# Kernel optimization log

Measured on AMD Instinct MI355X. Metric: run time of the kernel, lower is better.

## Reference

```python
import jax, jax.numpy as jnp
import numpy as np

T_MAX = 4
TOP_K = 4
TEMP = 1.0
THRESH = 0.99
EPS = 1e-6


def _to_c(x):
    return x[..., 0] + 1j * x[..., 1]


def _from_c(z):
    return jnp.stack([z.real, z.imag], axis=-1)


def _forward(psi, bank_keys, bank_vals, u_halt, W_halt, b_halt, head_mix, out_scale):
    B, T, d, _ = psi.shape
    H = bank_keys.shape[0]
    psi_flat = psi.reshape(B * T, d, 2)
    BT = psi_flat.shape[0]
    psi_h = jnp.broadcast_to(psi_flat[:, None], (BT, H, d, 2))
    cum = jnp.zeros((BT, H), psi.dtype)
    halted = jnp.zeros((BT, H), bool)
    cost = jnp.zeros((BT, H), psi.dtype)
    acc = jnp.zeros((BT, H, d, 2), psi.dtype)
    # normalized halt target vectors u (OrthoHalt)
    uc = _to_c(u_halt)  # [H,d] complex
    un = uc / jnp.sqrt(jnp.sum(uc.real**2 + uc.imag**2, -1, keepdims=True) + EPS)
    hidx = jnp.arange(H)
    for it in range(T_MAX):  # fixed small reasoning depth (structural loop)
        is_last = it == T_MAX - 1
        psi_pool = psi_h.mean(axis=1)                       # [BT,d,2]
        feat = psi_pool.reshape(BT, 2 * d)
        # effect-bank probe + top-k gather
        scores = jnp.einsum('bf,hnf->bhn', feat, bank_keys) / TEMP
        w = jax.nn.softmax(scores, axis=-1)                 # [BT,H,N]
        topw, topi = jax.lax.top_k(w, TOP_K)                # [BT,H,K]
        vecs = bank_vals[hidx[None, :, None], topi]         # [BT,H,K,d,2]
        U = _to_c(vecs) * topw[..., None].astype(jnp.complex64)  # weighted basis
        # rank-K Sasaki projection: Pi_F psi = A (A^H A)^{-1} A^H psi, A = U^T
        psic = _to_c(psi_h)                                 # [BT,H,d]
        m = jnp.einsum('bhkd,bhd->bhk', jnp.conj(U), psic)
        G = jnp.einsum('bhkd,bhjd->bhkj', jnp.conj(U), U)
        G = G + EPS * jnp.eye(TOP_K, dtype=G.dtype)
        coeff = jnp.linalg.solve(G, m[..., None])[..., 0]
        proj = jnp.einsum('bhkd,bhk->bhd', U, coeff)
        psi_next = _from_c(proj)
        # renormalize_psi
        sq = (psi_next[..., 0] ** 2 + psi_next[..., 1] ** 2).sum(-1, keepdims=True)
        psi_next = psi_next / jnp.sqrt(jnp.maximum(sq, 1e-6))[..., None]
        # OrthoHalt on pooled next state -> (alpha, beta, gamma) -> 3 logits
        pool_next = _to_c(psi_next.mean(axis=1))            # [BT,d]
        c = jnp.einsum('hd,bd->bh', jnp.conj(un), pool_next)
        ns = jnp.sum(pool_next.real**2 + pool_next.imag**2, -1)[:, None] + EPS
        alpha = (c.real**2 + c.imag**2) / ns
        beta = 1.0 - alpha
        gamma = c.real**2 / ns
        abg = jnp.stack([alpha, beta, gamma], -1)           # [BT,H,3]
        logits = jnp.einsum('bhi,hij->bhj', abg, W_halt) + b_halt
        probs = jax.nn.softmax(logits, -1)
        p_halt = probs[..., 0] + probs[..., 1]              # yes + no mass
        # ACT ponder update
        would = cum + p_halt
        halts_now = jnp.logical_or(would >= THRESH, is_last)
        active = jnp.logical_not(halted)
        weight = jnp.where(active, jnp.where(halts_now, 1.0 - cum, p_halt), 0.0)
        cost = cost + jnp.where(active, p_halt, 0.0)
        cum = jnp.where(jnp.logical_and(active, jnp.logical_not(halts_now)), would, cum)
        halted = jnp.logical_or(halted, jnp.logical_and(active, halts_now))
        acc = acc + weight[..., None, None] * psi_next
        psi_h = psi_next
    head_w = jax.nn.softmax(head_mix)[None, :, None, None]
    merged = (acc * head_w).sum(axis=1)                     # [BT,d,2]
    residual = merged - psi_flat
    psi_out = (psi_flat + out_scale * residual).reshape(B, T, d, 2)
    return psi_out, cost.mean()


def setup_inputs() -> dict:
    key = jax.random.key(0)
    ks = jax.random.split(key, 6)
    B, T, d, H, N = 2, 2048, 512, 4, 2048
    psi = jax.random.normal(ks[0], (B, T, d, 2), jnp.float32)
    psi = psi / jnp.sqrt(jnp.maximum((psi**2).sum((-1, -2), keepdims=True), 1e-6))
    bank_keys = 0.05 * jax.random.normal(ks[1], (H, N, 2 * d), jnp.float32)
    bank_vals = jax.random.normal(ks[2], (H, N, d, 2), jnp.float32)
    u_halt = jax.random.normal(ks[3], (H, d, 2), jnp.float32)
    W_halt = jax.random.normal(ks[4], (H, 3, 3), jnp.float32)
    b_halt = jnp.zeros((H, 3), jnp.float32)
    head_mix = jnp.zeros((H,), jnp.float32)
    out_scale = jnp.asarray(0.1, jnp.float32)
    return dict(psi=psi, bank_keys=bank_keys, bank_vals=bank_vals, u_halt=u_halt,
                W_halt=W_halt, b_halt=b_halt, head_mix=head_mix, out_scale=out_scale)


def reference(psi, bank_keys, bank_vals, u_halt, W_halt, b_halt, head_mix, out_scale):
    return _forward(psi, bank_keys, bank_vals, u_halt, W_halt, b_halt, head_mix, out_scale)
```

## Files before the change

kernel.cpp:

```cpp
#include <hip/hip_runtime.h>
#include <math.h>

#define HH 4
#define DD 512
#define FF 1024
#define NN 2048
#define KK 4
#define TMAXI 4
#define THRESHV 0.99f
#define EPSV 1e-6f

typedef unsigned short ushort_t;
typedef __attribute__((ext_vector_type(8))) __bf16 bf16x8;
typedef __attribute__((ext_vector_type(4))) float f32x4;
typedef __attribute__((ext_vector_type(4))) unsigned short us4;

__device__ __forceinline__ unsigned short f2bf(float x) {
    unsigned int u = __float_as_uint(x);
    unsigned int r = (u + 0x7FFF + ((u >> 16) & 1)) >> 16;
    return (unsigned short)r;
}

typedef __attribute__((address_space(3))) unsigned int lds_u32;
typedef __attribute__((address_space(1))) const unsigned int glb_u32;
__device__ __forceinline__ void gl_lds16(const void* g, void* s) {
    __builtin_amdgcn_global_load_lds((glb_u32*)g, (lds_u32*)s, 16, 0, 0);
}

__global__ void k_unorm(const float* __restrict__ u_halt, float* __restrict__ norm_inv) {
    __shared__ float red[256];
    int tid = threadIdx.x;
    for (int h = 0; h < HH; ++h) {
        float s = 0.f;
        for (int i = tid; i < FF; i += 256) { float v = u_halt[h * FF + i]; s += v * v; }
        red[tid] = s; __syncthreads();
        for (int off = 128; off > 0; off >>= 1) {
            if (tid < off) red[tid] += red[tid + off];
            __syncthreads();
        }
        if (tid == 0) norm_inv[h] = 1.0f / sqrtf(red[0] + EPSV);
        __syncthreads();
    }
}

__global__ void k_cvt_bf(const float* __restrict__ in, ushort_t* __restrict__ out, int total) {
    int i = blockIdx.x * 256 + threadIdx.x;
    if (i >= total) return;
    out[i] = f2bf(in[i]);
}

#define BM 128
#define BN 128
#define BKE 64
__global__ __launch_bounds__(256) void k_gemm_mfma(const ushort_t* __restrict__ A,
                                                   const ushort_t* __restrict__ B,
                                                   float* __restrict__ C) {
    __shared__ __align__(16) ushort_t As[BM * BKE];
    __shared__ __align__(16) ushort_t Bs[BN * BKE];
    int tid = threadIdx.x;
    int lane = tid & 63, w = tid >> 6;
    int row0 = blockIdx.y * BM, col0 = blockIdx.x * BN;

    int srow = lane >> 3;
    int schunk = (lane & 7) ^ srow;
    const ushort_t* gA = A + (size_t)(row0 + w * 32 + srow) * FF + schunk * 8;
    const ushort_t* gB = B + (size_t)(col0 + w * 32 + srow) * FF + schunk * 8;
    ushort_t* sA = As + (w * 32) * BKE;
    ushort_t* sB = Bs + (w * 32) * BKE;

    int fr = lane & 15;
    int q  = lane >> 4;
    int wr0 = (w >> 1) * 64, wc0 = (w & 1) * 64;

    f32x4 acc[4][4] = {};

    for (int kb = 0; kb < FF; kb += BKE) {
        #pragma unroll
        for (int i = 0; i < 4; i++) {
            gl_lds16(gA + kb + (size_t)(8 * i) * FF, sA + (8 * i) * BKE);
            gl_lds16(gB + kb + (size_t)(8 * i) * FF, sB + (8 * i) * BKE);
        }
        __syncthreads();
        bf16x8 af[2][4], bfv[2][4];
        #pragma unroll
        for (int hf = 0; hf < 2; hf++) {
            int ck = ((4 * hf + q) ^ (fr & 7)) * 8;
            #pragma unroll
            for (int i = 0; i < 4; i++) {
                af[hf][i]  = *(const bf16x8*)&As[(wr0 + 16 * i + fr) * BKE + ck];
                bfv[hf][i] = *(const bf16x8*)&Bs[(wc0 + 16 * i + fr) * BKE + ck];
            }
        }
        #pragma unroll
        for (int hf = 0; hf < 2; hf++)
            #pragma unroll
            for (int i = 0; i < 4; i++)
                #pragma unroll
                for (int j = 0; j < 4; j++)
                    acc[i][j] = __builtin_amdgcn_mfma_f32_16x16x32_bf16(af[hf][i], bfv[hf][j], acc[i][j], 0, 0, 0);
        __syncthreads();
    }

    int crow = (lane >> 4) * 4;
    int ccol = lane & 15;
    #pragma unroll
    for (int i = 0; i < 4; i++)
        #pragma unroll
        for (int r = 0; r < 4; r++) {
            float* Cr = C + (size_t)(row0 + wr0 + 16 * i + crow + r) * (HH * NN) + col0 + wc0 + ccol;
            #pragma unroll
            for (int j = 0; j < 4; j++) Cr[16 * j] = acc[i][j][r];
        }
}

__global__ __launch_bounds__(256) void k_softtop(const float* __restrict__ Sc,
                                                 float* __restrict__ topw, int* __restrict__ topi,
                                                 int row0) {
    int tid = threadIdx.x;
    int w = tid >> 6, lane = tid & 63;
    int g = blockIdx.x * 4 + w;
    int r = g >> 2;
    int h = g & 3;
    const float* S = Sc + (size_t)r * (HH * NN) + h * NN + lane * 4;
    float4 v[8];
    #pragma unroll
    for (int j = 0; j < 8; j++) v[j] = *(const float4*)(S + 256 * j);

    float bm = v[0].x;
    #pragma unroll
    for (int j = 0; j < 8; j++)
        bm = fmaxf(bm, fmaxf(fmaxf(v[j].x, v[j].y), fmaxf(v[j].z, v[j].w)));
    #pragma unroll
    for (int m = 1; m < 64; m <<= 1) bm = fmaxf(bm, __shfl_xor(bm, m, 64));

    float se = 0.f;
    #pragma unroll
    for (int j = 0; j < 8; j++)
        se += __expf(v[j].x - bm) + __expf(v[j].y - bm) + __expf(v[j].z - bm) + __expf(v[j].w - bm);
    #pragma unroll
    for (int m = 1; m < 64; m <<= 1) se += __shfl_xor(se, m, 64);
    float Zinv = __builtin_amdgcn_rcpf(se);

    int gbh = (row0 + r) * HH + h;
    int base = lane * 4;
    #pragma unroll
    for (int k = 0; k < KK; k++) {
        float bv = -INFINITY; int bi = NN;
        #pragma unroll
        for (int j = 0; j < 8; j++) {
            int n0 = 256 * j + base;
            if (v[j].x > bv) { bv = v[j].x; bi = n0; }
            if (v[j].y > bv) { bv = v[j].y; bi = n0 + 1; }
            if (v[j].z > bv) { bv = v[j].z; bi = n0 + 2; }
            if (v[j].w > bv) { bv = v[j].w; bi = n0 + 3; }
        }
        #pragma unroll
        for (int m = 1; m < 64; m <<= 1) {
            float ov = __shfl_xor(bv, m, 64);
            int   oi = __shfl_xor(bi, m, 64);
            if (ov > bv || (ov == bv && oi < bi)) { bv = ov; bi = oi; }
        }
        if (lane == 0) {
            topw[gbh * KK + k] = __expf(bv - bm) * Zinv;
            topi[gbh * KK + k] = bi;
        }
        if (k < KK - 1) {
            #pragma unroll
            for (int j = 0; j < 8; j++) {
                int n0 = 256 * j + base;
                if (n0     == bi) v[j].x = -INFINITY;
                if (n0 + 1 == bi) v[j].y = -INFINITY;
                if (n0 + 2 == bi) v[j].z = -INFINITY;
                if (n0 + 3 == bi) v[j].w = -INFINITY;
            }
        }
    }
}

__global__ __launch_bounds__(256) void k_fused(const float* __restrict__ psi,
                                               float* __restrict__ psi_h,
                                               const float* __restrict__ bank_vals,
                                               const float* __restrict__ topw,
                                               const int* __restrict__ topi,
                                               const float* __restrict__ u_halt,
                                               const float* __restrict__ norm_inv,
                                               const float* __restrict__ W_halt,
                                               const float* __restrict__ b_halt,
                                               const float* __restrict__ head_mix,
                                               float* __restrict__ merged,
                                               ushort_t* __restrict__ feat,
                                               float* __restrict__ cum,
                                               float* __restrict__ cost,
                                               int* __restrict__ halted,
                                               int first, int is_last) {
    __shared__ float Pn[HH][FF];
    __shared__ float xw[4][9];
    int b = blockIdx.x;
    int tid = threadIdx.x;
    int w = tid >> 6, lane = tid & 63;
    int bh = b * HH + w;

    float wk[KK]; int ix[KK];
    #pragma unroll
    for (int k = 0; k < KK; k++) { wk[k] = topw[bh * KK + k]; ix[k] = topi[bh * KK + k]; }

    const float* Pr = first ? (psi + (size_t)b * FF) : (psi_h + (size_t)bh * FF);
    float4 p4[4], v4[KK][4];
    #pragma unroll
    for (int c = 0; c < 4; c++) p4[c] = *(const float4*)(Pr + lane * 16 + 4 * c);
    #pragma unroll
    for (int k = 0; k < KK; k++) {
        const float* Vp = bank_vals + ((size_t)(w * NN) + ix[k]) * FF + lane * 16;
        #pragma unroll
        for (int c = 0; c < 4; c++) v4[k][c] = *(const float4*)(Vp + 4 * c);
    }

    float part[24];
    #pragma unroll
    for (int t = 0; t < 24; t++) part[t] = 0.f;
    #pragma unroll
    for (int c = 0; c < 4; c++) {
        #pragma unroll
        for (int e = 0; e < 2; e++) {
            float prr = e ? p4[c].z : p4[c].x;
            float pii = e ? p4[c].w : p4[c].y;
            float vr[KK], vi[KK];
            #pragma unroll
            for (int k = 0; k < KK; k++) {
                vr[k] = e ? v4[k][c].z : v4[k][c].x;
                vi[k] = e ? v4[k][c].w : v4[k][c].y;
            }
            #pragma unroll
            for (int k = 0; k < KK; k++) {
                part[2 * k]     += vr[k] * prr + vi[k] * pii;
                part[2 * k + 1] += vr[k] * pii - vi[k] * prr;
                part[8 + k]     += vr[k] * vr[k] + vi[k] * vi[k];
            }
            int t = 12;
            #pragma unroll
            for (int k = 0; k < KK; k++)
                #pragma unroll
                for (int j = k + 1; j < KK; j++) {
                    part[t]     += vr[k] * vr[j] + vi[k] * vi[j];
                    part[t + 1] += vr[k] * vi[j] - vi[k] * vr[j];
                    t += 2;
                }
        }
    }
    #pragma unroll
    for (int m = 1; m < 64; m <<= 1)
        #pragma unroll
        for (int t = 0; t < 24; t++) part[t] += __shfl_xor(part[t], m, 64);

    float mr[KK], mi[KK], Gr[KK][KK], Gi[KK][KK];
    #pragma unroll
    for (int k = 0; k < KK; k++) {
        mr[k] = part[2 * k] * wk[k];
        mi[k] = part[2 * k + 1] * wk[k];
        Gr[k][k] = part[8 + k] * wk[k] * wk[k] + EPSV;
        Gi[k][k] = 0.f;
    }
    {
        int t = 12;
        #pragma unroll
        for (int k = 0; k < KK; k++)
            #pragma unroll
            for (int j = k + 1; j < KK; j++) {
                float s = wk[k] * wk[j];
                Gr[k][j] = part[t] * s;  Gi[k][j] = part[t + 1] * s;
                Gr[j][k] = Gr[k][j];     Gi[j][k] = -Gi[k][j];
                t += 2;
            }
    }

    float Lr[KK][KK], Li[KK][KK];
    #pragma unroll
    for (int j = 0; j < KK; j++) {
        float s = Gr[j][j];
        #pragma unroll
        for (int p = 0; p < KK; p++) if (p < j) s -= Lr[j][p] * Lr[j][p] + Li[j][p] * Li[j][p];
        float ljj = sqrtf(fmaxf(s, 1e-30f));
        Lr[j][j] = ljj; Li[j][j] = 0.f;
        float inv = 1.0f / ljj;
        #pragma unroll
        for (int k = 0; k < KK; k++) {
            if (k > j) {
                float ar = Gr[k][j], ai = Gi[k][j];
                #pragma unroll
                for (int p = 0; p < KK; p++) if (p < j) {
                    ar -= Lr[k][p] * Lr[j][p] + Li[k][p] * Li[j][p];
                    ai -= Li[k][p] * Lr[j][p] - Lr[k][p] * Li[j][p];
                }
                Lr[k][j] = ar * inv; Li[k][j] = ai * inv;
            }
        }
    }
    float yr[KK], yi[KK];
    #pragma unroll
    for (int j = 0; j < KK; j++) {
        float ar = mr[j], ai = mi[j];
        #pragma unroll
        for (int p = 0; p < KK; p++) if (p < j) {
            ar -= Lr[j][p] * yr[p] - Li[j][p] * yi[p];
            ai -= Lr[j][p] * yi[p] + Li[j][p] * yr[p];
        }
        float inv = 1.0f / Lr[j][j];
        yr[j] = ar * inv; yi[j] = ai * inv;
    }
    float xr[KK], xi2[KK];
    #pragma unroll
    for (int j = KK - 1; j >= 0; j--) {
        float ar = yr[j], ai = yi[j];
        #pragma unroll
        for (int p = 0; p < KK; p++) if (p > j) {
            ar -= Lr[p][j] * xr[p] + Li[p][j] * xi2[p];
            ai -= Lr[p][j] * xi2[p] - Li[p][j] * xr[p];
        }
        float inv = 1.0f / Lr[j][j];
        xr[j] = ar * inv; xi2[j] = ai * inv;
    }
    float cxr[KK], cxi[KK];
    #pragma unroll
    for (int k = 0; k < KK; k++) { cxr[k] = xr[k] * wk[k]; cxi[k] = xi2[k] * wk[k]; }

    float4 pj[4];
    float sqp = 0.f;
    #pragma unroll
    for (int c = 0; c < 4; c++) {
        float ar0 = 0.f, ai0 = 0.f, ar1 = 0.f, ai1 = 0.f;
        #pragma unroll
        for (int k = 0; k < KK; k++) {
            ar0 += v4[k][c].x * cxr[k] - v4[k][c].y * cxi[k];
            ai0 += v4[k][c].x * cxi[k] + v4[k][c].y * cxr[k];
            ar1 += v4[k][c].z * cxr[k] - v4[k][c].w * cxi[k];
            ai1 += v4[k][c].z * cxi[k] + v4[k][c].w * cxr[k];
        }
        pj[c].x = ar0; pj[c].y = ai0; pj[c].z = ar1; pj[c].w = ai1;
        sqp += ar0 * ar0 + ai0 * ai0 + ar1 * ar1 + ai1 * ai1;
    }
    #pragma unroll
    for (int m = 1; m < 64; m <<= 1) sqp += __shfl_xor(sqp, m, 64);
    float rn = 1.0f / sqrtf(fmaxf(sqp, 1e-6f));

    float* Pdst = psi_h + (size_t)bh * FF + lane * 16;
    #pragma unroll
    for (int c = 0; c < 4; c++) {
        float4 o; o.x = pj[c].x * rn; o.y = pj[c].y * rn; o.z = pj[c].z * rn; o.w = pj[c].w * rn;
        *(float4*)(Pdst + 4 * c) = o;
        *(float4*)&Pn[w][lane * 16 + 4 * c] = o;
    }
    __syncthreads();

    int t4 = tid * 4;
    float4 a0 = *(const float4*)&Pn[0][t4];
    float4 a1 = *(const float4*)&Pn[1][t4];
    float4 a2 = *(const float4*)&Pn[2][t4];
    float4 a3 = *(const float4*)&Pn[3][t4];
    float4 pool;
    pool.x = 0.25f * (a0.x + a1.x + a2.x + a3.x);
    pool.y = 0.25f * (a0.y + a1.y + a2.y + a3.y);
    pool.z = 0.25f * (a0.z + a1.z + a2.z + a3.z);
    pool.w = 0.25f * (a0.w + a1.w + a2.w + a3.w);

    float pt[9];
    #pragma unroll
    for (int h = 0; h < HH; h++) {
        float4 u = *(const float4*)&u_halt[h * FF + t4];
        pt[2 * h]     = u.x * pool.x + u.y * pool.y + u.z * pool.z + u.w * pool.w;
        pt[2 * h + 1] = u.x * pool.y - u.y * pool.x + u.z * pool.w - u.w * pool.z;
    }
    pt[8] = pool.x * pool.x + pool.y * pool.y + pool.z * pool.z + pool.w * pool.w;
    #pragma unroll
    for (int m = 1; m < 64; m <<= 1)
        #pragma unroll
        for (int t = 0; t < 9; t++) pt[t] += __shfl_xor(pt[t], m, 64);
    if (lane == 0) {
        #pragma unroll
        for (int t = 0; t < 9; t++) xw[w][t] = pt[t];
    }
    __syncthreads();
    float red[9];
    #pragma unroll
    for (int t = 0; t < 9; t++) red[t] = xw[0][t] + xw[1][t] + xw[2][t] + xw[3][t];
    float ns = red[8] + EPSV;

    float hm0 = head_mix[0], hm1 = head_mix[1], hm2 = head_mix[2], hm3 = head_mix[3];
    float hmx = fmaxf(fmaxf(hm0, hm1), fmaxf(hm2, hm3));
    float he[4] = {expf(hm0 - hmx), expf(hm1 - hmx), expf(hm2 - hmx), expf(hm3 - hmx)};
    float hsum = he[0] + he[1] + he[2] + he[3];

    float wgt[4], addc[4], newcum[4]; int newhl[4];
    int idxb = b * HH;
    #pragma unroll
    for (int h = 0; h < HH; h++) {
        float cr = red[2 * h] * norm_inv[h], ci = red[2 * h + 1] * norm_inv[h];
        float alpha = (cr * cr + ci * ci) / ns;
        float beta = 1.0f - alpha;
        float gamma = cr * cr / ns;
        float lg[3];
        #pragma unroll
        for (int j = 0; j < 3; j++)
            lg[j] = alpha * W_halt[(h * 3 + 0) * 3 + j] + beta * W_halt[(h * 3 + 1) * 3 + j] +
                    gamma * W_halt[(h * 3 + 2) * 3 + j] + b_halt[h * 3 + j];
        float mx = fmaxf(lg[0], fmaxf(lg[1], lg[2]));
        float e0 = expf(lg[0] - mx), e1 = expf(lg[1] - mx), e2 = expf(lg[2] - mx);
        float p_halt = (e0 + e1) / (e0 + e1 + e2);
        float cm = cum[idxb + h];
        int hl = halted[idxb + h];
        float would = cm + p_halt;
        int halts_now = (would >= THRESHV) || is_last;
        int active = hl ? 0 : 1;
        wgt[h]  = active ? (halts_now ? (1.0f - cm) : p_halt) : 0.0f;
        addc[h] = active ? p_halt : 0.0f;
        newcum[h] = (active && !halts_now) ? would : cm;
        newhl[h]  = hl || (active && halts_now);
    }
    __syncthreads();
    if (tid < HH) {
        cost[idxb + tid] += addc[tid];
        cum[idxb + tid] = newcum[tid];
        halted[idxb + tid] = newhl[tid];
    }
    float hwv[4];
    #pragma unroll
    for (int h = 0; h < HH; h++) hwv[h] = (he[h] / hsum) * wgt[h];

    size_t mo = (size_t)b * FF + t4;
    float4 m4 = *(const float4*)&merged[mo];
    m4.x += hwv[0] * a0.x + hwv[1] * a1.x + hwv[2] * a2.x + hwv[3] * a3.x;
    m4.y += hwv[0] * a0.y + hwv[1] * a1.y + hwv[2] * a2.y + hwv[3] * a3.y;
    m4.z += hwv[0] * a0.z + hwv[1] * a1.z + hwv[2] * a2.z + hwv[3] * a3.z;
    m4.w += hwv[0] * a0.w + hwv[1] * a1.w + hwv[2] * a2.w + hwv[3] * a3.w;
    *(float4*)&merged[mo] = m4;

    us4 fb;
    fb.x = f2bf(pool.x); fb.y = f2bf(pool.y); fb.z = f2bf(pool.z); fb.w = f2bf(pool.w);
    *(us4*)&feat[mo] = fb;
}

__global__ void k_out(const float* __restrict__ psi, const float* __restrict__ merged,
                      const float* __restrict__ out_scale, float* __restrict__ out, int total) {
    int i = blockIdx.x * 256 + threadIdx.x;
    if (i >= total) return;
    float p = psi[i];
    out[i] = p + out_scale[0] * (merged[i] - p);
}

__global__ void k_costmean(const float* __restrict__ cost, float* __restrict__ out, int n) {
    __shared__ float red[256];
    int tid = threadIdx.x;
    float s = 0.f;
    for (int i = tid; i < n; i += 256) s += cost[i];
    red[tid] = s; __syncthreads();
    for (int off = 128; off > 0; off >>= 1) {
        if (tid < off) red[tid] += red[tid + off];
        __syncthreads();
    }
    if (tid == 0) out[0] = red[0] / (float)n;
}

extern "C" void kernel_launch(void* const* d_in, const int* in_sizes, int n_in,
                              void* d_out, int out_size, void* d_ws, size_t ws_size,
                              hipStream_t stream) {
    const float* psi       = (const float*)d_in[0];
    const float* bank_keys = (const float*)d_in[1];
    const float* bank_vals = (const float*)d_in[2];
    const float* u_halt    = (const float*)d_in[3];
    const float* W_halt    = (const float*)d_in[4];
    const float* b_halt    = (const float*)d_in[5];
    const float* head_mix  = (const float*)d_in[6];
    const float* out_scale = (const float*)d_in[7];
    float* out = (float*)d_out;

    const int BT = in_sizes[0] / FF;

    float* ws = (float*)d_ws;
    size_t off = 0;
    float* psi_h  = ws + off; off += (size_t)BT * HH * FF;
    float* merged = ws + off; off += (size_t)BT * FF;
    float* cum    = ws + off; off += (size_t)BT * HH;
    float* costv  = ws + off; off += (size_t)BT * HH;
    int*   halted = (int*)(ws + off); off += (size_t)BT * HH;
    float* topw   = ws + off; off += (size_t)BT * HH * KK;
    int*   topi   = (int*)(ws + off); off += (size_t)BT * HH * KK;
    float* norminv = ws + off; off += 16;
    ushort_t* feat_bf = (ushort_t*)(ws + off); off += (size_t)BT * FF / 2;
    ushort_t* keys_bf = (ushort_t*)(ws + off); off += (size_t)HH * NN * FF / 2;
    float* scores = ws + off;
    size_t fixed = off;

    size_t ws_floats = ws_size / 4;
    int RC = BT;
    while (RC > 128 && fixed + (size_t)RC * HH * NN > ws_floats) RC >>= 1;
    int nchunks = BT / RC;

    hipMemsetAsync(merged, 0, ((size_t)BT * FF + 3 * (size_t)BT * HH) * sizeof(float), stream);
    k_unorm<<<1, 256, 0, stream>>>(u_halt, norminv);
    int tot_keys = HH * NN * FF;
    k_cvt_bf<<<(tot_keys + 255) / 256, 256, 0, stream>>>(bank_keys, keys_bf, tot_keys);
    int tot_bf = BT * FF;
    k_cvt_bf<<<(tot_bf + 255) / 256, 256, 0, stream>>>(psi, feat_bf, tot_bf);

    for (int it = 0; it < TMAXI; ++it) {
        for (int c = 0; c < nchunks; ++c) {
            k_gemm_mfma<<<dim3((HH * NN) / BN, RC / BM), 256, 0, stream>>>(
                feat_bf + (size_t)c * RC * FF, keys_bf, scores);
            k_softtop<<<dim3((RC * HH) / 4), 256, 0, stream>>>(scores, topw, topi, c * RC);
        }
        k_fused<<<BT, 256, 0, stream>>>(psi, psi_h, bank_vals, topw, topi, u_halt, norminv,
                                        W_halt, b_halt, head_mix, merged, feat_bf,
                                        cum, costv, halted,
                                        (it == 0) ? 1 : 0, (it == TMAXI - 1) ? 1 : 0);
    }
    k_out<<<(tot_bf + 255) / 256, 256, 0, stream>>>(psi, merged, out_scale, out, tot_bf);
    k_costmean<<<1, 256, 0, stream>>>(costv, out + tot_bf, BT * HH);
}
```

Before: 1.119 ms.

## Fuse softmax/top-k partials into GEMM epilogue, merge segments in small kernel

The GEMM epilogue no longer writes the full score matrix. Each 128-column tile instead computes a per-row local max, sum-exp and top-4 with shuffles and LDS, and writes a small segment record. A new merge kernel combines the 16 segments per (row, head) into the global softmax normalizer and top-4 weights and indices. This removes the large score write and re-read and the chunking loop, at the cost of extra epilogue work and LDS reuse inside the GEMM.

```diff
diff --git a/kernel.cpp b/kernel.cpp
--- a/kernel.cpp
+++ b/kernel.cpp
@@ -54,7 +54,7 @@
 #define BKE 64
 __global__ __launch_bounds__(256) void k_gemm_mfma(const ushort_t* __restrict__ A,
                                                    const ushort_t* __restrict__ B,
-                                                   float* __restrict__ C) {
+                                                   float* __restrict__ segbuf) {
     __shared__ __align__(16) ushort_t As[BM * BKE];
     __shared__ __align__(16) ushort_t Bs[BN * BKE];
     int tid = threadIdx.x;
@@ -101,80 +101,122 @@
         __syncthreads();
     }
 
-    int crow = (lane >> 4) * 4;
-    int ccol = lane & 15;
-    #pragma unroll
-    for (int i = 0; i < 4; i++)
+    float* seg = (float*)As;
+    int nb0 = (col0 & (NN - 1)) + wc0 + fr;
+    #pragma unroll
+    for (int i = 0; i < 4; i++) {
         #pragma unroll
         for (int r = 0; r < 4; r++) {
-            float* Cr = C + (size_t)(row0 + wr0 + 16 * i + crow + r) * (HH * NN) + col0 + wc0 + ccol;
-            #pragma unroll
-            for (int j = 0; j < 4; j++) Cr[16 * j] = acc[i][j][r];
-        }
-}
-
-__global__ __launch_bounds__(256) void k_softtop(const float* __restrict__ Sc,
-                                                 float* __restrict__ topw, int* __restrict__ topi,
-                                                 int row0) {
-    int tid = threadIdx.x;
-    int w = tid >> 6, lane = tid & 63;
-    int g = blockIdx.x * 4 + w;
-    int r = g >> 2;
-    int h = g & 3;
-    const float* S = Sc + (size_t)r * (HH * NN) + h * NN + lane * 4;
-    float4 v[8];
-    #pragma unroll
-    for (int j = 0; j < 8; j++) v[j] = *(const float4*)(S + 256 * j);
-
-    float bm = v[0].x;
-    #pragma unroll
-    for (int j = 0; j < 8; j++)
-        bm = fmaxf(bm, fmaxf(fmaxf(v[j].x, v[j].y), fmaxf(v[j].z, v[j].w)));
-    #pragma unroll
-    for (int m = 1; m < 64; m <<= 1) bm = fmaxf(bm, __shfl_xor(bm, m, 64));
-
-    float se = 0.f;
-    #pragma unroll
-    for (int j = 0; j < 8; j++)
-        se += __expf(v[j].x - bm) + __expf(v[j].y - bm) + __expf(v[j].z - bm) + __expf(v[j].w - bm);
-    #pragma unroll
-    for (int m = 1; m < 64; m <<= 1) se += __shfl_xor(se, m, 64);
-    float Zinv = __builtin_amdgcn_rcpf(se);
-
-    int gbh = (row0 + r) * HH + h;
-    int base = lane * 4;
-    #pragma unroll
-    for (int k = 0; k < KK; k++) {
-        float bv = -INFINITY; int bi = NN;
-        #pragma unroll
-        for (int j = 0; j < 8; j++) {
-            int n0 = 256 * j + base;
-            if (v[j].x > bv) { bv = v[j].x; bi = n0; }
-            if (v[j].y > bv) { bv = v[j].y; bi = n0 + 1; }
-            if (v[j].z > bv) { bv = v[j].z; bi = n0 + 2; }
-            if (v[j].w > bv) { bv = v[j].w; bi = n0 + 3; }
-        }
-        #pragma unroll
-        for (int m = 1; m < 64; m <<= 1) {
-            float ov = __shfl_xor(bv, m, 64);
-            int   oi = __shfl_xor(bi, m, 64);
-            if (ov > bv || (ov == bv && oi < bi)) { bv = ov; bi = oi; }
-        }
-        if (lane == 0) {
-            topw[gbh * KK + k] = __expf(bv - bm) * Zinv;
-            topi[gbh * KK + k] = bi;
-        }
-        if (k < KK - 1) {
-            #pragma unroll
-            for (int j = 0; j < 8; j++) {
-                int n0 = 256 * j + base;
-                if (n0     == bi) v[j].x = -INFINITY;
-                if (n0 + 1 == bi) v[j].y = -INFINITY;
-                if (n0 + 2 == bi) v[j].z = -INFINITY;
-                if (n0 + 3 == bi) v[j].w = -INFINITY;
-            }
-        }
-    }
+            float c0 = acc[i][0][r], c1 = acc[i][1][r], c2 = acc[i][2][r], c3 = acc[i][3][r];
+            float mx = fmaxf(fmaxf(c0, c1), fmaxf(c2, c3));
+            #pragma unroll
+            for (int m = 1; m < 16; m <<= 1) mx = fmaxf(mx, __shfl_xor(mx, m, 64));
+            float s = __expf(c0 - mx) + __expf(c1 - mx) + __expf(c2 - mx) + __expf(c3 - mx);
+            #pragma unroll
+            for (int m = 1; m < 16; m <<= 1) s += __shfl_xor(s, m, 64);
+            float tv[4]; int ti[4];
+            #pragma unroll
+            for (int k = 0; k < 4; k++) {
+                float bv = c0; int bi = nb0;
+                if (c1 > bv) { bv = c1; bi = nb0 + 16; }
+                if (c2 > bv) { bv = c2; bi = nb0 + 32; }
+                if (c3 > bv) { bv = c3; bi = nb0 + 48; }
+                #pragma unroll
+                for (int m = 1; m < 16; m <<= 1) {
+                    float ov = __shfl_xor(bv, m, 64); int oi = __shfl_xor(bi, m, 64);
+                    if (ov > bv || (ov == bv && oi < bi)) { bv = ov; bi = oi; }
+                }
+                tv[k] = bv; ti[k] = bi;
+                if (k < 3) {
+                    if (bi == nb0) c0 = -INFINITY;
+                    else if (bi == nb0 + 16) c1 = -INFINITY;
+                    else if (bi == nb0 + 32) c2 = -INFINITY;
+                    else if (bi == nb0 + 48) c3 = -INFINITY;
+                }
+            }
+            if (fr == 0) {
+                int rr = wr0 + 16 * i + 4 * q + r;
+                float* d = &seg[(rr * 2 + (w & 1)) * 10];
+                d[0] = mx; d[1] = s;
+                d[2] = tv[0]; d[3] = tv[1]; d[4] = tv[2]; d[5] = tv[3];
+                int* di = (int*)d;
+                di[6] = ti[0]; di[7] = ti[1]; di[8] = ti[2]; di[9] = ti[3];
+            }
+        }
+    }
+    __syncthreads();
+
+    if (tid < 128) {
+        float* d0 = &seg[(tid * 2 + 0) * 10];
+        float* d1 = &seg[(tid * 2 + 1) * 10];
+        float am = d0[0], as = d0[1], bm = d1[0], bs = d1[1];
+        float gm = fmaxf(am, bm);
+        float gs = as * __expf(am - gm) + bs * __expf(bm - gm);
+        float a0 = d0[2], a1 = d0[3], a2 = d0[4], a3 = d0[5];
+        float b0 = d1[2], b1 = d1[3], b2 = d1[4], b3 = d1[5];
+        int* e0 = (int*)d0; int* e1 = (int*)d1;
+        int x0 = e0[6], x1 = e0[7], x2 = e0[8], x3 = e0[9];
+        int y0 = e1[6], y1 = e1[7], y2 = e1[8], y3 = e1[9];
+        float nv0, nv1, nv2, nv3; int ni0, ni1, ni2, ni3;
+        #pragma unroll
+        for (int k = 0; k < 4; k++) {
+            bool ta = (a0 >= b0);
+            float nv = ta ? a0 : b0; int ni = ta ? x0 : y0;
+            if (k == 0) { nv0 = nv; ni0 = ni; }
+            else if (k == 1) { nv1 = nv; ni1 = ni; }
+            else if (k == 2) { nv2 = nv; ni2 = ni; }
+            else { nv3 = nv; ni3 = ni; }
+            if (ta) { a0 = a1; a1 = a2; a2 = a3; a3 = -INFINITY; x0 = x1; x1 = x2; x2 = x3; }
+            else    { b0 = b1; b1 = b2; b2 = b3; b3 = -INFINITY; y0 = y1; y1 = y2; y2 = y3; }
+        }
+        int grow = row0 + tid;
+        int head = col0 >> 11;
+        int segid = (col0 & (NN - 1)) >> 7;
+        float* o = segbuf + ((size_t)(grow * HH + head) * 16 + segid) * 10;
+        o[0] = gm; o[1] = gs;
+        o[2] = nv0; o[3] = nv1; o[4] = nv2; o[5] = nv3;
+        o[6] = __int_as_float(ni0); o[7] = __int_as_float(ni1);
+        o[8] = __int_as_float(ni2); o[9] = __int_as_float(ni3);
+    }
+}
+
+__global__ __launch_bounds__(256) void k_mergetop(const float* __restrict__ segb,
+                                                  float* __restrict__ topw,
+                                                  int* __restrict__ topi) {
+    int g = blockIdx.x * 256 + threadIdx.x;
+    const float* base = segb + (size_t)g * 160;
+    float gm = base[0], gs = base[1];
+    float c0 = base[2], c1 = base[3], c2 = base[4], c3 = base[5];
+    int i0 = __float_as_int(base[6]), i1 = __float_as_int(base[7]);
+    int i2 = __float_as_int(base[8]), i3 = __float_as_int(base[9]);
+    for (int s = 1; s < 16; s++) {
+        const float* d = base + s * 10;
+        float sm = d[0], ss = d[1];
+        float b0 = d[2], b1 = d[3], b2 = d[4], b3 = d[5];
+        int y0 = __float_as_int(d[6]), y1 = __float_as_int(d[7]);
+        int y2 = __float_as_int(d[8]), y3 = __float_as_int(d[9]);
+        float ngm = fmaxf(gm, sm);
+        gs = gs * __expf(gm - ngm) + ss * __expf(sm - ngm);
+        gm = ngm;
+        float a0 = c0, a1 = c1, a2 = c2, a3 = c3;
+        int x0 = i0, x1 = i1, x2 = i2, x3 = i3;
+        #pragma unroll
+        for (int k = 0; k < 4; k++) {
+            bool ta = (a0 >= b0);
+            float nv = ta ? a0 : b0; int ni = ta ? x0 : y0;
+            if (k == 0) { c0 = nv; i0 = ni; }
+            else if (k == 1) { c1 = nv; i1 = ni; }
+            else if (k == 2) { c2 = nv; i2 = ni; }
+            else { c3 = nv; i3 = ni; }
+            if (ta) { a0 = a1; a1 = a2; a2 = a3; a3 = -INFINITY; x0 = x1; x1 = x2; x2 = x3; }
+            else    { b0 = b1; b1 = b2; b2 = b3; b3 = -INFINITY; y0 = y1; y1 = y2; y2 = y3; }
+        }
+    }
+    float zi = __builtin_amdgcn_rcpf(gs);
+    topw[g * 4 + 0] = __expf(c0 - gm) * zi; topi[g * 4 + 0] = i0;
+    topw[g * 4 + 1] = __expf(c1 - gm) * zi; topi[g * 4 + 1] = i1;
+    topw[g * 4 + 2] = __expf(c2 - gm) * zi; topi[g * 4 + 2] = i2;
+    topw[g * 4 + 3] = __expf(c3 - gm) * zi; topi[g * 4 + 3] = i3;
 }
 
 __global__ __launch_bounds__(256) void k_fused(const float* __restrict__ psi,
@@ -486,13 +528,7 @@
     float* norminv = ws + off; off += 16;
     ushort_t* feat_bf = (ushort_t*)(ws + off); off += (size_t)BT * FF / 2;
     ushort_t* keys_bf = (ushort_t*)(ws + off); off += (size_t)HH * NN * FF / 2;
-    float* scores = ws + off;
-    size_t fixed = off;
-
-    size_t ws_floats = ws_size / 4;
-    int RC = BT;
-    while (RC > 128 && fixed + (size_t)RC * HH * NN > ws_floats) RC >>= 1;
-    int nchunks = BT / RC;
+    float* segbuf = ws + off; off += (size_t)BT * HH * 16 * 10;
 
     hipMemsetAsync(merged, 0, ((size_t)BT * FF + 3 * (size_t)BT * HH) * sizeof(float), stream);
     k_unorm<<<1, 256, 0, stream>>>(u_halt, norminv);
@@ -502,11 +538,8 @@
     k_cvt_bf<<<(tot_bf + 255) / 256, 256, 0, stream>>>(psi, feat_bf, tot_bf);
 
     for (int it = 0; it < TMAXI; ++it) {
-        for (int c = 0; c < nchunks; ++c) {
-            k_gemm_mfma<<<dim3((HH * NN) / BN, RC / BM), 256, 0, stream>>>(
-                feat_bf + (size_t)c * RC * FF, keys_bf, scores);
-            k_softtop<<<dim3((RC * HH) / 4), 256, 0, stream>>>(scores, topw, topi, c * RC);
-        }
+        k_gemm_mfma<<<dim3((HH * NN) / BN, BT / BM), 256, 0, stream>>>(feat_bf, keys_bf, segbuf);
+        k_mergetop<<<(BT * HH) / 256, 256, 0, stream>>>(segbuf, topw, topi);
         k_fused<<<BT, 256, 0, stream>>>(psi, psi_h, bank_vals, topw, topi, u_halt, norminv,
                                         W_halt, b_halt, head_mix, merged, feat_bf,
                                         cum, costv, halted,
```

Result: slower. 1.489 ms (+33.1%).
